# Performance work log

Measured on AMD Instinct MI355X. Metric: run time of the kernel, lower is better.

## Reference

```python
import jax, jax.numpy as jnp
import numpy as np

S = 8192        # seq_length
H2 = 1024       # 2 * lstm_hidden_size
A = 2048        # attention_hidden_size
E = 768         # embedding_dim == pos_embedding_dim


def _bahdanau_weights(sentence, length, ctx, W_s, b_s, W_c, b_c, v, b_v):
    # sentence: [1, S, H2], ctx: [1, E_ctx]
    u = jnp.einsum('bsh,ha->bsa', sentence, W_s) + b_s \
        + (ctx @ W_c + b_c)[:, None, :]                    # [1, S, A]
    e = jnp.einsum('bsa,a->bs', jnp.tanh(u), v) + b_v       # [1, S]
    mask = jnp.arange(S)[None, :] >= length[:, None]        # [1, S] key mask
    e = jnp.where(mask, -jnp.inf, e)
    all_inf = jnp.all(mask, axis=1)                         # [1]
    # guard fully-masked rows so softmax stays finite, then zero them (matches torch)
    e_safe = jnp.where(all_inf[:, None], jnp.zeros_like(e), e)
    w = jax.nn.softmax(e_safe, axis=1)
    return jnp.where(all_inf[:, None], 0.0, w)              # [1, S]


def setup_inputs() -> dict:
    key = jax.random.key(0)
    ks = jax.random.split(key, 24)
    f = jax.random.normal
    sc_s = 1.0 / np.sqrt(H2)
    sc_c = 1.0 / np.sqrt(E)
    sc_v = 1.0 / np.sqrt(A)
    inp = {
        'sentence': f(ks[0], (1, S, H2), jnp.float32),
        'length': jax.random.randint(ks[1], (1,), 0, S),
        'pos_embedding': f(ks[2], (1, E), jnp.float32),
        'cardinal_phrase_embedding': f(ks[3], (1, E), jnp.float32),
        'headline_embedding': f(ks[4], (1, E), jnp.float32),
    }
    i = 5
    for tag in ('p', 'c', 'h'):
        inp[f'W_sent_{tag}'] = f(ks[i], (H2, A), jnp.float32) * sc_s; i += 1
        inp[f'b_sent_{tag}'] = f(ks[i], (A,), jnp.float32) * sc_s; i += 1
        inp[f'W_ctx_{tag}'] = f(ks[i], (E, A), jnp.float32) * sc_c; i += 1
        inp[f'b_ctx_{tag}'] = f(ks[i], (A,), jnp.float32) * sc_c; i += 1
        inp[f'v_{tag}'] = f(ks[i], (A,), jnp.float32) * sc_v; i += 1
        inp[f'bv_{tag}'] = f(ks[i], (), jnp.float32) * sc_v; i += 1
    return inp


def reference(sentence, length, pos_embedding, cardinal_phrase_embedding,
              headline_embedding,
              W_sent_p, b_sent_p, W_ctx_p, b_ctx_p, v_p, bv_p,
              W_sent_c, b_sent_c, W_ctx_c, b_ctx_c, v_c, bv_c,
              W_sent_h, b_sent_h, W_ctx_h, b_ctx_h, v_h, bv_h):
    w_pos = _bahdanau_weights(sentence, length, pos_embedding,
                              W_sent_p, b_sent_p, W_ctx_p, b_ctx_p, v_p, bv_p)
    w_card = _bahdanau_weights(sentence, length, cardinal_phrase_embedding,
                               W_sent_c, b_sent_c, W_ctx_c, b_ctx_c, v_c, bv_c)
    w_head = _bahdanau_weights(sentence, length, headline_embedding,
                               W_sent_h, b_sent_h, W_ctx_h, b_ctx_h, v_h, bv_h)
    fused = (w_pos + w_card + w_head) / 3.0                 # [1, S]
    return jnp.einsum('bs,bsh->bh', fused, sentence)        # [1, H2]
```

## Files before the change

kernel.cpp:

```cpp
#include <hip/hip_runtime.h>
#include <hip/hip_bf16.h>
#include <stdint.h>


namespace {

constexpr int S = 8192;
constexpr int H = 1024;
constexpr int A = 2048;
constexpr int E = 768;

typedef __bf16 bf16x8 __attribute__((ext_vector_type(8)));
typedef float f32x4 __attribute__((ext_vector_type(4)));

__device__ __forceinline__ void gl_lds16(const void* g, void* l) {
  __builtin_amdgcn_global_load_lds(
      (const __attribute__((address_space(1))) void*)g,
      (__attribute__((address_space(3))) void*)l, 16, 0, 0);
}

__global__ __launch_bounds__(256)
void k_prep(const float* __restrict__ sentence, __bf16* __restrict__ sentB,
            const float* __restrict__ Wp, const float* __restrict__ Wc_s,
            const float* __restrict__ Wh, __bf16* __restrict__ WtB,
            const float* __restrict__ ctx_p, const float* __restrict__ ctx_c,
            const float* __restrict__ ctx_h,
            const float* __restrict__ Wcx_p, const float* __restrict__ Wcx_c,
            const float* __restrict__ Wcx_h,
            const float* __restrict__ bs_p, const float* __restrict__ bs_c,
            const float* __restrict__ bs_h,
            const float* __restrict__ bc_p, const float* __restrict__ bc_c,
            const float* __restrict__ bc_h,
            float* __restrict__ ctxb,
            const int* __restrict__ length, float* __restrict__ out, int n_out) {
  __shared__ float tile[64][65];
  int b = blockIdx.x;
  int t = threadIdx.x;

  if (b < 4096) {
    int len = min(max(length[0], 0), S);
    int lenp = (len + 63) & ~63;
    if (b * 2 >= lenp) return;
    int g = b * 256 + t;
    const float4* s4 = (const float4*)sentence + (size_t)g * 2;
    float4 a = s4[0], c = s4[1];
    bf16x8 o;
    o[0] = (__bf16)a.x; o[1] = (__bf16)a.y; o[2] = (__bf16)a.z; o[3] = (__bf16)a.w;
    o[4] = (__bf16)c.x; o[5] = (__bf16)c.y; o[6] = (__bf16)c.z; o[7] = (__bf16)c.w;
    *((bf16x8*)sentB + g) = o;
  } else if (b < 5632) {
    int r = b - 4096;
    int head = r >> 9; r &= 511;
    const float* W = head == 0 ? Wp : (head == 1 ? Wc_s : Wh);
    __bf16* dst = WtB + (size_t)head * A * H;
    int a0 = (r & 31) * 64;
    int k0 = (r >> 5) * 64;
#pragma unroll
    for (int i = 0; i < 16; ++i) {
      int idx = t + i * 256;
      int rr = idx >> 6, cc = idx & 63;
      tile[cc][rr] = W[(size_t)(k0 + rr) * A + a0 + cc];
    }
    __syncthreads();
#pragma unroll
    for (int i = 0; i < 16; ++i) {
      int idx = t + i * 256;
      int al = idx >> 6, kl = idx & 63;
      dst[(size_t)(a0 + al) * H + k0 + kl] = (__bf16)tile[al][kl];
    }
  } else if (b < 6208) {
    int r = b - 5632;
    int head = r / 192; r %= 192;
    int ablk = r & 7;
    int echk = r >> 3;
    const float* ctx = head == 0 ? ctx_p : (head == 1 ? ctx_c : ctx_h);
    const float* Wc  = head == 0 ? Wcx_p : (head == 1 ? Wcx_c : Wcx_h);
    int a = ablk * 256 + t;
    float s = 0.f;
    int e0 = echk * 32;
#pragma unroll 8
    for (int e = e0; e < e0 + 32; ++e) s = fmaf(ctx[e], Wc[(size_t)e * A + a], s);
    if (echk == 0) {
      const float* bs = head == 0 ? bs_p : (head == 1 ? bs_c : bs_h);
      const float* bc = head == 0 ? bc_p : (head == 1 ? bc_c : bc_h);
      s += bs[a] + bc[a];
    }
    atomicAdd(&ctxb[head * A + a], s);
  } else {
    float4 z = {0.f, 0.f, 0.f, 0.f};
    for (int i = t; i * 4 < n_out; i += 256) ((float4*)out)[i] = z;
  }
}

__global__ __launch_bounds__(256)
void k_gemm_e(const __bf16* __restrict__ sentB, const __bf16* __restrict__ WtB,
              const float* __restrict__ ctxb,
              const float* __restrict__ v_p, const float* __restrict__ v_c,
              const float* __restrict__ v_h,
              const int* __restrict__ length, float* __restrict__ e_out) {
  int m0 = blockIdx.x * 64;
  int len = min(max(length[0], 0), S);
  if (m0 >= len) return;
  int n0 = blockIdx.y * 128;
  int head = blockIdx.z;
  const float* v  = head == 0 ? v_p : (head == 1 ? v_c : v_h);
  const __bf16* Wt = WtB + (size_t)head * A * H;
  const float* cb = ctxb + head * A;
  float* e_h = e_out + head * S;

  __shared__ __align__(16) __bf16 lsA[3 * 2048];
  __shared__ __align__(16) __bf16 lsB[3 * 4096];
  __shared__ float e_part[64];

  int tid = threadIdx.x;
  if (tid < 64) e_part[tid] = 0.f;

  int lane = tid & 63;
  int wave = tid >> 6;
  int wm = wave >> 1, wn = wave & 1;
  int quad = lane >> 4, l16 = lane & 15;

  f32x4 acc[2][4];
#pragma unroll
  for (int i = 0; i < 2; ++i)
#pragma unroll
    for (int j = 0; j < 4; ++j) acc[i][j] = (f32x4){0.f, 0.f, 0.f, 0.f};

  const __bf16* gA0 = sentB + (size_t)(m0 + (tid >> 2)) * H + ((tid & 3) * 8);
  const __bf16* gB0 = Wt + (size_t)(n0 + (tid >> 2)) * H + ((tid & 3) * 8);
  const __bf16* gB1 = gB0 + (size_t)64 * H;

#define STAGE(bufi, kk)                                           \
  do {                                                            \
    gl_lds16(gA0 + (kk), lsA + (bufi) * 2048 + tid * 8);          \
    gl_lds16(gB0 + (kk), lsB + (bufi) * 4096 + tid * 8);          \
    gl_lds16(gB1 + (kk), lsB + (bufi) * 4096 + 2048 + tid * 8);   \
  } while (0)

#define COMPUTE(bufi)                                                                          \
  do {                                                                                         \
    bf16x8 af[2], bfv[4];                                                                      \
    _Pragma("unroll")                                                                          \
    for (int i = 0; i < 2; ++i)                                                                \
      af[i] = *(const bf16x8*)&lsA[(bufi) * 2048 + (wm * 32 + i * 16 + l16) * 32 + quad * 8];  \
    _Pragma("unroll")                                                                          \
    for (int j = 0; j < 4; ++j)                                                                \
      bfv[j] = *(const bf16x8*)&lsB[(bufi) * 4096 + (wn * 64 + j * 16 + l16) * 32 + quad * 8]; \
    _Pragma("unroll")                                                                          \
    for (int i = 0; i < 2; ++i)                                                                \
      _Pragma("unroll")                                                                        \
      for (int j = 0; j < 4; ++j)                                                              \
        acc[i][j] = __builtin_amdgcn_mfma_f32_16x16x32_bf16(af[i], bfv[j], acc[i][j], 0, 0, 0);\
  } while (0)

  STAGE(0, 0);
  STAGE(1, 32);
  int cur = 0, pf = 2;
#pragma unroll 1
  for (int t = 0; t < 31; ++t) {
    asm volatile("s_waitcnt vmcnt(3)");
    __builtin_amdgcn_s_barrier();
    __builtin_amdgcn_sched_barrier(0);
    if (t < 30) STAGE(pf, (t + 2) * 32);
    COMPUTE(cur);
    cur = cur == 2 ? 0 : cur + 1;
    pf = pf == 2 ? 0 : pf + 1;
  }
  asm volatile("s_waitcnt vmcnt(0)");
  __builtin_amdgcn_s_barrier();
  __builtin_amdgcn_sched_barrier(0);
  COMPUTE(cur);

#undef STAGE
#undef COMPUTE

  float vj[4], cbj[4];
#pragma unroll
  for (int j = 0; j < 4; ++j) {
    int col = n0 + wn * 64 + j * 16 + l16;
    vj[j] = v[col];
    cbj[j] = cb[col];
  }
#pragma unroll
  for (int i = 0; i < 2; ++i) {
#pragma unroll
    for (int r = 0; r < 4; ++r) {
      float p = 0.f;
#pragma unroll
      for (int j = 0; j < 4; ++j) {
        float u = acc[i][j][r] + cbj[j];
        float ex = __expf(2.f * u);
        float th = 1.f - 2.f / (ex + 1.f);
        p = fmaf(th, vj[j], p);
      }
      p += __shfl_xor(p, 1);
      p += __shfl_xor(p, 2);
      p += __shfl_xor(p, 4);
      p += __shfl_xor(p, 8);
      if (l16 == 0) atomicAdd(&e_part[wm * 32 + i * 16 + quad * 4 + r], p);
    }
  }
  __syncthreads();
  if (tid < 64) atomicAdd(&e_h[m0 + tid], e_part[tid]);
}

__global__ void k_out(const float* __restrict__ sent, const float* __restrict__ e_arr,
                      const int* __restrict__ length, float* __restrict__ out) {
  int len = min(max(length[0], 0), S);
  int r0 = blockIdx.x * 16;
  if (r0 >= len) return;
  int tid = threadIdx.x;

  __shared__ float red[3][4];
  __shared__ float sstat[6];
  __shared__ float wrow[16];

#pragma unroll
  for (int h = 0; h < 3; ++h) {
    const float* e_h = e_arr + h * S;
    float m = -3.4e38f;
    for (int s = tid; s < len; s += 256) m = fmaxf(m, e_h[s]);
#pragma unroll
    for (int o = 32; o >= 1; o >>= 1) m = fmaxf(m, __shfl_xor(m, o));
    if ((tid & 63) == 0) red[h][tid >> 6] = m;
  }
  __syncthreads();
  if (tid < 3) sstat[tid * 2] = fmaxf(fmaxf(red[tid][0], red[tid][1]),
                                      fmaxf(red[tid][2], red[tid][3]));
  __syncthreads();
#pragma unroll
  for (int h = 0; h < 3; ++h) {
    const float* e_h = e_arr + h * S;
    float mm = sstat[h * 2];
    float ss = 0.f;
    for (int s = tid; s < len; s += 256) ss += __expf(e_h[s] - mm);
#pragma unroll
    for (int o = 32; o >= 1; o >>= 1) ss += __shfl_xor(ss, o);
    if ((tid & 63) == 0) red[h][tid >> 6] = ss;
  }
  __syncthreads();
  if (tid < 3) sstat[tid * 2 + 1] = red[tid][0] + red[tid][1] + red[tid][2] + red[tid][3];
  __syncthreads();

  if (tid < 16 && r0 + tid < len) {
    int r = r0 + tid;
    wrow[tid] = (__expf(e_arr[r] - sstat[0]) / sstat[1] +
                 __expf(e_arr[S + r] - sstat[2]) / sstat[3] +
                 __expf(e_arr[2 * S + r] - sstat[4]) / sstat[5]) * (1.f / 3.f);
  }
  __syncthreads();

  int col = tid * 4;
  int rend = min(r0 + 16, len);
  float4 acc = {0.f, 0.f, 0.f, 0.f};
  for (int r = r0; r < rend; ++r) {
    float w = wrow[r - r0];
    float4 x = *(const float4*)(sent + (size_t)r * H + col);
    acc.x = fmaf(w, x.x, acc.x);
    acc.y = fmaf(w, x.y, acc.y);
    acc.z = fmaf(w, x.z, acc.z);
    acc.w = fmaf(w, x.w, acc.w);
  }
  atomicAdd(&out[col + 0], acc.x);
  atomicAdd(&out[col + 1], acc.y);
  atomicAdd(&out[col + 2], acc.z);
  atomicAdd(&out[col + 3], acc.w);
}

}

extern "C" void kernel_launch(void* const* d_in, const int* in_sizes, int n_in,
                              void* d_out, int out_size, void* d_ws, size_t ws_size,
                              hipStream_t stream) {
  const float* sentence = (const float*)d_in[0];
  const int* length     = (const int*)d_in[1];
  const float* ctx_p = (const float*)d_in[2];
  const float* ctx_c = (const float*)d_in[3];
  const float* ctx_h = (const float*)d_in[4];
  const float* W_s[3] = {(const float*)d_in[5],  (const float*)d_in[11], (const float*)d_in[17]};
  const float* b_s[3] = {(const float*)d_in[6],  (const float*)d_in[12], (const float*)d_in[18]};
  const float* W_c[3] = {(const float*)d_in[7],  (const float*)d_in[13], (const float*)d_in[19]};
  const float* b_c[3] = {(const float*)d_in[8],  (const float*)d_in[14], (const float*)d_in[20]};
  const float* v_[3]  = {(const float*)d_in[9],  (const float*)d_in[15], (const float*)d_in[21]};
  float* out = (float*)d_out;

  char* ws = (char*)d_ws;
  __bf16* sentB = (__bf16*)(ws);
  __bf16* WtB   = (__bf16*)(ws + 16777216);
  float* ctxb   = (float*)(ws + 29360128);
  float* e_arr  = (float*)(ws + 29384704);

  hipMemsetAsync(ctxb, 0, (A * 3 + S * 3) * sizeof(float), stream);

  k_prep<<<6209, 256, 0, stream>>>(sentence, sentB,
                                   W_s[0], W_s[1], W_s[2], WtB,
                                   ctx_p, ctx_c, ctx_h,
                                   W_c[0], W_c[1], W_c[2],
                                   b_s[0], b_s[1], b_s[2],
                                   b_c[0], b_c[1], b_c[2], ctxb,
                                   length, out, out_size);
  k_gemm_e<<<dim3(S / 64, A / 128, 3), 256, 0, stream>>>(sentB, WtB, ctxb,
                                                         v_[0], v_[1], v_[2], length, e_arr);
  k_out<<<S / 16, 256, 0, stream>>>(sentence, e_arr, length, out);
}
```

Measured before the change: 212.8 us.

## Fuse context projection into GEMM prologue, deepen pipeline to four stages, drop memset

The context-vector projection (ctx @ W_ctx + biases) moves out of the prep kernel's atomic blocks and into each GEMM block. Each block computes its 128 columns while its first three prefetch stages are in flight, which removes the hipMemsetAsync call and the atomics. The GEMM's LDS pipeline goes from three to four buffers, and zeroing of the e array and output is folded into a small grid-strided part of the prep kernel. The cost is redundant context work: every m-block recomputes a 768-deep dot product per column, about 128× duplicated loads of W_ctx. The larger LDS footprint may also reduce occupancy.

```diff
diff --git a/kernel.cpp b/kernel.cpp
--- a/kernel.cpp
+++ b/kernel.cpp
@@ -23,15 +23,7 @@
 void k_prep(const float* __restrict__ sentence, __bf16* __restrict__ sentB,
             const float* __restrict__ Wp, const float* __restrict__ Wc_s,
             const float* __restrict__ Wh, __bf16* __restrict__ WtB,
-            const float* __restrict__ ctx_p, const float* __restrict__ ctx_c,
-            const float* __restrict__ ctx_h,
-            const float* __restrict__ Wcx_p, const float* __restrict__ Wcx_c,
-            const float* __restrict__ Wcx_h,
-            const float* __restrict__ bs_p, const float* __restrict__ bs_c,
-            const float* __restrict__ bs_h,
-            const float* __restrict__ bc_p, const float* __restrict__ bc_c,
-            const float* __restrict__ bc_h,
-            float* __restrict__ ctxb,
+            float* __restrict__ e_arr,
             const int* __restrict__ length, float* __restrict__ out, int n_out) {
   __shared__ float tile[64][65];
   int b = blockIdx.x;
@@ -68,33 +60,27 @@
       int al = idx >> 6, kl = idx & 63;
       dst[(size_t)(a0 + al) * H + k0 + kl] = (__bf16)tile[al][kl];
     }
-  } else if (b < 6208) {
-    int r = b - 5632;
-    int head = r / 192; r %= 192;
-    int ablk = r & 7;
-    int echk = r >> 3;
-    const float* ctx = head == 0 ? ctx_p : (head == 1 ? ctx_c : ctx_h);
-    const float* Wc  = head == 0 ? Wcx_p : (head == 1 ? Wcx_c : Wcx_h);
-    int a = ablk * 256 + t;
-    float s = 0.f;
-    int e0 = echk * 32;
-#pragma unroll 8
-    for (int e = e0; e < e0 + 32; ++e) s = fmaf(ctx[e], Wc[(size_t)e * A + a], s);
-    if (echk == 0) {
-      const float* bs = head == 0 ? bs_p : (head == 1 ? bs_c : bs_h);
-      const float* bc = head == 0 ? bc_p : (head == 1 ? bc_c : bc_h);
-      s += bs[a] + bc[a];
+  } else {
+    int idx = (b - 5632) * 256 + t;
+    float4 z = {0.f, 0.f, 0.f, 0.f};
+    int total = 6144 + (n_out >> 2);
+    for (int i = idx; i < total; i += 2048) {
+      if (i < 6144) ((float4*)e_arr)[i] = z;
+      else ((float4*)out)[i - 6144] = z;
     }
-    atomicAdd(&ctxb[head * A + a], s);
-  } else {
-    float4 z = {0.f, 0.f, 0.f, 0.f};
-    for (int i = t; i * 4 < n_out; i += 256) ((float4*)out)[i] = z;
   }
 }
 
 __global__ __launch_bounds__(256)
 void k_gemm_e(const __bf16* __restrict__ sentB, const __bf16* __restrict__ WtB,
-              const float* __restrict__ ctxb,
+              const float* __restrict__ ctx_p, const float* __restrict__ ctx_c,
+              const float* __restrict__ ctx_h,
+              const float* __restrict__ Wcx_p, const float* __restrict__ Wcx_c,
+              const float* __restrict__ Wcx_h,
+              const float* __restrict__ bs_p, const float* __restrict__ bs_c,
+              const float* __restrict__ bs_h,
+              const float* __restrict__ bc_p, const float* __restrict__ bc_c,
+              const float* __restrict__ bc_h,
               const float* __restrict__ v_p, const float* __restrict__ v_c,
               const float* __restrict__ v_h,
               const int* __restrict__ length, float* __restrict__ e_out) {
@@ -105,11 +91,11 @@
   int head = blockIdx.z;
   const float* v  = head == 0 ? v_p : (head == 1 ? v_c : v_h);
   const __bf16* Wt = WtB + (size_t)head * A * H;
-  const float* cb = ctxb + head * A;
   float* e_h = e_out + head * S;
 
-  __shared__ __align__(16) __bf16 lsA[3 * 2048];
-  __shared__ __align__(16) __bf16 lsB[3 * 4096];
+  __shared__ __align__(16) __bf16 lsA[4 * 2048];
+  __shared__ __align__(16) __bf16 lsB[4 * 4096];
+  __shared__ float cb_part[256];
   __shared__ float e_part[64];
 
   int tid = threadIdx.x;
@@ -155,31 +141,51 @@
 
   STAGE(0, 0);
   STAGE(1, 32);
-  int cur = 0, pf = 2;
+  STAGE(2, 64);
+  {
+    const float* ctx = head == 0 ? ctx_p : (head == 1 ? ctx_c : ctx_h);
+    const float* Wc  = head == 0 ? Wcx_p : (head == 1 ? Wcx_c : Wcx_h);
+    int col = n0 + (tid & 127);
+    int e0 = (tid >> 7) * (E / 2);
+    float s = 0.f;
+#pragma unroll 8
+    for (int e = e0; e < e0 + E / 2; ++e) s = fmaf(ctx[e], Wc[(size_t)e * A + col], s);
+    cb_part[tid] = s;
+  }
+
 #pragma unroll 1
-  for (int t = 0; t < 31; ++t) {
-    asm volatile("s_waitcnt vmcnt(3)");
+  for (int t = 0; t < 29; ++t) {
+    asm volatile("s_waitcnt vmcnt(6)");
     __builtin_amdgcn_s_barrier();
     __builtin_amdgcn_sched_barrier(0);
-    if (t < 30) STAGE(pf, (t + 2) * 32);
-    COMPUTE(cur);
-    cur = cur == 2 ? 0 : cur + 1;
-    pf = pf == 2 ? 0 : pf + 1;
-  }
+    STAGE((t + 3) & 3, (t + 3) * 32);
+    COMPUTE(t & 3);
+  }
+  asm volatile("s_waitcnt vmcnt(6)");
+  __builtin_amdgcn_s_barrier();
+  __builtin_amdgcn_sched_barrier(0);
+  COMPUTE(1);
+  asm volatile("s_waitcnt vmcnt(3)");
+  __builtin_amdgcn_s_barrier();
+  __builtin_amdgcn_sched_barrier(0);
+  COMPUTE(2);
   asm volatile("s_waitcnt vmcnt(0)");
   __builtin_amdgcn_s_barrier();
   __builtin_amdgcn_sched_barrier(0);
-  COMPUTE(cur);
+  COMPUTE(3);
 
 #undef STAGE
 #undef COMPUTE
 
+  const float* bs = head == 0 ? bs_p : (head == 1 ? bs_c : bs_h);
+  const float* bc = head == 0 ? bc_p : (head == 1 ? bc_c : bc_h);
   float vj[4], cbj[4];
 #pragma unroll
   for (int j = 0; j < 4; ++j) {
-    int col = n0 + wn * 64 + j * 16 + l16;
+    int cl = wn * 64 + j * 16 + l16;
+    int col = n0 + cl;
     vj[j] = v[col];
-    cbj[j] = cb[col];
+    cbj[j] = cb_part[cl] + cb_part[128 + cl] + bs[col] + bc[col];
   }
 #pragma unroll
   for (int i = 0; i < 2; ++i) {
@@ -287,19 +293,17 @@
   char* ws = (char*)d_ws;
   __bf16* sentB = (__bf16*)(ws);
   __bf16* WtB   = (__bf16*)(ws + 16777216);
-  float* ctxb   = (float*)(ws + 29360128);
   float* e_arr  = (float*)(ws + 29384704);
 
-  hipMemsetAsync(ctxb, 0, (A * 3 + S * 3) * sizeof(float), stream);
-
-  k_prep<<<6209, 256, 0, stream>>>(sentence, sentB,
+  k_prep<<<5640, 256, 0, stream>>>(sentence, sentB,
                                    W_s[0], W_s[1], W_s[2], WtB,
-                                   ctx_p, ctx_c, ctx_h,
-                                   W_c[0], W_c[1], W_c[2],
-                                   b_s[0], b_s[1], b_s[2],
-                                   b_c[0], b_c[1], b_c[2], ctxb,
-                                   length, out, out_size);
-  k_gemm_e<<<dim3(S / 64, A / 128, 3), 256, 0, stream>>>(sentB, WtB, ctxb,
-                                                         v_[0], v_[1], v_[2], length, e_arr);
+                                   e_arr, length, out, out_size);
+  k_gemm_e<<<dim3(S / 64, A / 128, 3), 256, 0, stream>>>(
+      sentB, WtB,
+      ctx_p, ctx_c, ctx_h,
+      W_c[0], W_c[1], W_c[2],
+      b_s[0], b_s[1], b_s[2],
+      b_c[0], b_c[1], b_c[2],
+      v_[0], v_[1], v_[2], length, e_arr);
   k_out<<<S / 16, 256, 0, stream>>>(sentence, e_arr, length, out);
 }
```

Measured after the change: 251.5 us. 1.18x slower.
